# Kernel tuning notes

Measured on AMD Instinct MI355X. Metric: run time of the kernel, lower is better.

Reference implementation:

```python
import jax, jax.numpy as jnp
import numpy as np

CHUNK_DIVISOR = 4


def setup_inputs() -> dict:
    key = jax.random.key(0)
    k1, k2 = jax.random.split(key)
    B, L, D = 4, 8192, 1024
    hidden_states = jax.random.normal(k1, (B, L, D), dtype=jnp.float32)
    boundary_mask = jax.random.randint(k2, (B, L), 0, 2).astype(jnp.bool_)
    return {"hidden_states": hidden_states, "boundary_mask": boundary_mask}


def reference(hidden_states, boundary_mask):
    # hidden_states: [B, L, D]; boundary_mask: [B, L] bool
    B, L, D = hidden_states.shape
    max_chunks = L // CHUNK_DIVISOR
    num_chunks = jnp.minimum(boundary_mask.sum(axis=-1), max_chunks)  # [B]
    # selected positions get key = t, unselected get key = t + L -> sort compacts selected to front
    token_idx = jnp.arange(L)[None, :] + (~boundary_mask).astype(jnp.int32) * L  # [B, L]
    sorted_idx = jnp.argsort(token_idx, axis=1)
    take_idx = sorted_idx[:, :max_chunks]  # [B, max_chunks]
    chunked = jnp.take_along_axis(hidden_states, take_idx[:, :, None], axis=1)  # [B, max_chunks, D]
    pad_mask = jnp.arange(max_chunks)[None, :] < num_chunks[:, None]  # [B, max_chunks]
    chunked = chunked * pad_mask[:, :, None].astype(chunked.dtype)
    return chunked, pad_mask, take_idx
```

## Files before the change

### kernel.cpp

```cpp
#include <hip/hip_runtime.h>

#define BB 4
#define LL 8192
#define DD 1024
#define MAXC (LL / 4)

__global__ __launch_bounds__(256) void chunk_scan_kernel(
    const int* __restrict__ mask,
    int*       __restrict__ tk_int,
    int*       __restrict__ nchunks,
    float*     __restrict__ out_pad,
    float*     __restrict__ out_tk)
{
    const int b = blockIdx.x;
    const int t = threadIdx.x;
    constexpr int PER = LL / 256;

    const int* m = mask + (size_t)b * LL;
    int local[PER];
    const int4* m4 = reinterpret_cast<const int4*>(m + t * PER);
#pragma unroll
    for (int j = 0; j < PER / 4; ++j) {
        int4 v = m4[j];
        local[4 * j + 0] = v.x;
        local[4 * j + 1] = v.y;
        local[4 * j + 2] = v.z;
        local[4 * j + 3] = v.w;
    }
    int s = 0;
#pragma unroll
    for (int j = 0; j < PER; ++j) s += local[j];

    __shared__ int sums[256];
    sums[t] = s;
    __syncthreads();
    for (int off = 1; off < 256; off <<= 1) {
        int v = 0;
        if (t >= off) v = sums[t - off];
        __syncthreads();
        if (t >= off) sums[t] += v;
        __syncthreads();
    }
    const int total = sums[255];
    const int excl  = sums[t] - s;
    const int nc    = (total < MAXC) ? total : MAXC;

    int pb = excl;
    const int base = t * PER;
#pragma unroll
    for (int j = 0; j < PER; ++j) {
        const int i = base + j;
        int r;
        if (local[j]) {
            r = pb;
            ++pb;
        } else {
            r = total + (i - pb);
        }
        if (r < MAXC) {
            const int o = b * MAXC + r;
            tk_int[o]  = i;
            out_tk[o]  = (float)i;
            out_pad[o] = (r < nc) ? 1.0f : 0.0f;
        }
    }
    if (t == 0) nchunks[b] = nc;
}

__global__ __launch_bounds__(256) void chunk_gather_kernel(
    const float* __restrict__ hs,
    const int*   __restrict__ tk_int,
    const int*   __restrict__ nchunks,
    float*       __restrict__ out)
{
    const int row = blockIdx.x;
    const int b   = row >> 11;
    const int r   = row & (MAXC - 1);
    const int t   = threadIdx.x;

    float4* o = reinterpret_cast<float4*>(out + (size_t)row * DD);
    if (r < nchunks[b]) {
        const int i = tk_int[row];
        const float4* src =
            reinterpret_cast<const float4*>(hs + ((size_t)b * LL + i) * DD);
        o[t] = src[t];
    } else {
        o[t] = make_float4(0.f, 0.f, 0.f, 0.f);
    }
}

extern "C" void kernel_launch(void* const* d_in, const int* in_sizes, int n_in,
                              void* d_out, int out_size, void* d_ws, size_t ws_size,
                              hipStream_t stream) {
    const float* hs   = (const float*)d_in[0];
    const int*   mask = (const int*)d_in[1];

    float* out = (float*)d_out;
    float* out_chunk = out;
    float* out_pad   = out + (size_t)BB * MAXC * DD;
    float* out_tk    = out_pad + (size_t)BB * MAXC;

    int* tk_int  = (int*)d_ws;
    int* nchunks = tk_int + BB * MAXC;

    chunk_scan_kernel<<<BB, 256, 0, stream>>>(mask, tk_int, nchunks,
                                              out_pad, out_tk);
    chunk_gather_kernel<<<BB * MAXC, 256, 0, stream>>>(hs, tk_int, nchunks,
                                                       out_chunk);
}
```

Measured before the change: 22.44 us.

## Use wave-shuffle scan and gather four rows per block with nontemporal access

The scan kernel grows to 1024 threads per batch and replaces the multi-barrier shared-memory Hillis-Steele scan with a wavefront shuffle scan plus a 16-entry cross-wave sum, which cuts the number of block-wide barriers. The gather kernel now copies four rows per block, issuing all loads before the stores, and uses nontemporal loads and stores. This reduces the block count and gives each thread more memory operations in flight. Nontemporal hints may change cache behaviour, and the larger blocks leave fewer scan blocks resident per CU.

After: 20.87 us. 1.08x faster.

```diff
diff --git a/kernel.cpp b/kernel.cpp
--- a/kernel.cpp
+++ b/kernel.cpp
@@ -5,7 +5,10 @@
 #define DD 1024
 #define MAXC (LL / 4)
 
-__global__ __launch_bounds__(256) void chunk_scan_kernel(
+typedef float f32x4 __attribute__((ext_vector_type(4)));
+typedef int   i32x4 __attribute__((ext_vector_type(4)));
+
+__global__ __launch_bounds__(1024) void chunk_scan_kernel(
     const int* __restrict__ mask,
     int*       __restrict__ tk_int,
     int*       __restrict__ nchunks,
@@ -14,49 +17,48 @@
 {
     const int b = blockIdx.x;
     const int t = threadIdx.x;
-    constexpr int PER = LL / 256;
+    constexpr int PER = LL / 1024;
 
     const int* m = mask + (size_t)b * LL;
-    int local[PER];
-    const int4* m4 = reinterpret_cast<const int4*>(m + t * PER);
-#pragma unroll
-    for (int j = 0; j < PER / 4; ++j) {
-        int4 v = m4[j];
-        local[4 * j + 0] = v.x;
-        local[4 * j + 1] = v.y;
-        local[4 * j + 2] = v.z;
-        local[4 * j + 3] = v.w;
-    }
+    const i32x4* m4 = reinterpret_cast<const i32x4*>(m + t * PER);
+    i32x4 v0 = m4[0];
+    i32x4 v1 = m4[1];
+    int local[PER] = {v0.x, v0.y, v0.z, v0.w, v1.x, v1.y, v1.z, v1.w};
+
     int s = 0;
 #pragma unroll
     for (int j = 0; j < PER; ++j) s += local[j];
 
-    __shared__ int sums[256];
-    sums[t] = s;
+    const int lane = t & 63;
+    const int wid  = t >> 6;
+    int inc = s;
+#pragma unroll
+    for (int off = 1; off < 64; off <<= 1) {
+        int n = __shfl_up(inc, off, 64);
+        if (lane >= off) inc += n;
+    }
+
+    __shared__ int wsum[16];
+    if (lane == 63) wsum[wid] = inc;
     __syncthreads();
-    for (int off = 1; off < 256; off <<= 1) {
-        int v = 0;
-        if (t >= off) v = sums[t - off];
-        __syncthreads();
-        if (t >= off) sums[t] += v;
-        __syncthreads();
+
+    int wpre = 0, total = 0;
+#pragma unroll
+    for (int w = 0; w < 16; ++w) {
+        int x = wsum[w];
+        total += x;
+        wpre += (w < wid) ? x : 0;
     }
-    const int total = sums[255];
-    const int excl  = sums[t] - s;
-    const int nc    = (total < MAXC) ? total : MAXC;
+    const int excl = wpre + inc - s;
+    const int nc   = (total < MAXC) ? total : MAXC;
 
     int pb = excl;
     const int base = t * PER;
 #pragma unroll
     for (int j = 0; j < PER; ++j) {
         const int i = base + j;
-        int r;
-        if (local[j]) {
-            r = pb;
-            ++pb;
-        } else {
-            r = total + (i - pb);
-        }
+        const int r = local[j] ? pb : (total + (i - pb));
+        pb += local[j];
         if (r < MAXC) {
             const int o = b * MAXC + r;
             tk_int[o]  = i;
@@ -73,19 +75,30 @@
     const int*   __restrict__ nchunks,
     float*       __restrict__ out)
 {
-    const int row = blockIdx.x;
-    const int b   = row >> 11;
-    const int r   = row & (MAXC - 1);
-    const int t   = threadIdx.x;
+    const int t    = threadIdx.x;
+    const int row0 = blockIdx.x * 4;
+    const int b    = row0 >> 11;
+    const int nc   = nchunks[b];
 
-    float4* o = reinterpret_cast<float4*>(out + (size_t)row * DD);
-    if (r < nchunks[b]) {
-        const int i = tk_int[row];
-        const float4* src =
-            reinterpret_cast<const float4*>(hs + ((size_t)b * LL + i) * DD);
-        o[t] = src[t];
-    } else {
-        o[t] = make_float4(0.f, 0.f, 0.f, 0.f);
+    f32x4 vals[4];
+#pragma unroll
+    for (int k = 0; k < 4; ++k) {
+        const int row = row0 + k;
+        const int r   = row & (MAXC - 1);
+        if (r < nc) {
+            const int i = tk_int[row];
+            const f32x4* src =
+                reinterpret_cast<const f32x4*>(hs + ((size_t)b * LL + i) * DD);
+            vals[k] = __builtin_nontemporal_load(&src[t]);
+        } else {
+            vals[k] = (f32x4){0.f, 0.f, 0.f, 0.f};
+        }
+    }
+
+    f32x4* o = reinterpret_cast<f32x4*>(out + (size_t)row0 * DD);
+#pragma unroll
+    for (int k = 0; k < 4; ++k) {
+        __builtin_nontemporal_store(vals[k], &o[k * 256 + t]);
     }
 }
 
@@ -103,8 +116,8 @@
     int* tk_int  = (int*)d_ws;
     int* nchunks = tk_int + BB * MAXC;
 
-    chunk_scan_kernel<<<BB, 256, 0, stream>>>(mask, tk_int, nchunks,
-                                              out_pad, out_tk);
-    chunk_gather_kernel<<<BB * MAXC, 256, 0, stream>>>(hs, tk_int, nchunks,
-                                                       out_chunk);
+    chunk_scan_kernel<<<BB, 1024, 0, stream>>>(mask, tk_int, nchunks,
+                                               out_pad, out_tk);
+    chunk_gather_kernel<<<BB * MAXC / 4, 256, 0, stream>>>(hs, tk_int, nchunks,
+                                                           out_chunk);
 }
```
